# Kernel optimization log

Hardware: AMD Instinct MI355X
Metric: run time of the kernel (lower is better)

The kernel has to match this reference:

```python
import jax, jax.numpy as jnp
import numpy as np

NUM_CAPSULE = 16
DIM_CAPSULE = 64
ROUTINGS = 3
T_EPS = 1e-7


def setup_inputs() -> dict:
    key = jax.random.key(0)
    k1, k2 = jax.random.split(key)
    x = jax.random.normal(k1, (64, 512, 768), dtype=jnp.float32)
    # xavier-normal-ish init for W: [1, input_dim_capsule, num_capsule*dim_capsule]
    fan_in, fan_out = 768, NUM_CAPSULE * DIM_CAPSULE
    std = float(np.sqrt(2.0 / (fan_in + fan_out)))
    W = jax.random.normal(k2, (1, 768, NUM_CAPSULE * DIM_CAPSULE), dtype=jnp.float32) * std
    return {"x": x, "W": W}


def _squash(v, eps=T_EPS):
    # NOTE: this module's 'squash' is pure L2 normalization with eps, not the
    # classic (s^2/(1+s^2)) squash.
    s2 = jnp.sum(v * v, axis=-1, keepdims=True)
    return v / jnp.sqrt(s2 + eps)


def reference(x, W):
    B, In, _ = x.shape
    # u_hat: [B, In, num*dim] -> [B, num, In, dim]
    u = jnp.matmul(x, W).reshape(B, In, NUM_CAPSULE, DIM_CAPSULE).transpose(0, 2, 1, 3)
    b = jnp.zeros((B, NUM_CAPSULE, In), dtype=u.dtype)  # routing logits
    outputs = None
    for i in range(ROUTINGS):
        # torch code softmaxes over the num_capsule axis (after permute dance)
        c = jax.nn.softmax(b, axis=1)  # [B, num, In]
        outputs = _squash(jnp.einsum('bij,bijk->bik', c, u))  # [B, num, dim]
        if i < ROUTINGS - 1:
            b = jnp.einsum('bik,bijk->bij', outputs, u)  # [B, num, In]
    return outputs
```

## Files before the change

### kernel.cpp

```cpp
#include <hip/hip_runtime.h>
#include <hip/hip_bf16.h>
#include <stdint.h>

#define BATCH 64
#define IN_CAPS 512
#define NCAP 16
#define DCAP 64
#define GN (NCAP * DCAP)
#define GM (BATCH * IN_CAPS)
#define GK 768

typedef __bf16 bf16;
typedef __attribute__((ext_vector_type(8))) __bf16 bf16x8;
typedef __attribute__((ext_vector_type(4))) float f32x4;

__device__ inline void async16(const bf16* g, bf16* l) {
    __builtin_amdgcn_global_load_lds(
        (__attribute__((address_space(1))) void*)g,
        (__attribute__((address_space(3))) void*)l, 16, 0, 0);
}

__global__ __launch_bounds__(256) void k_convX2(const float* __restrict__ X,
                                                bf16* __restrict__ Xb,
                                                float* __restrict__ XS) {
    __shared__ float ls[GK];
    const int tid = threadIdx.x;
    ls[tid] = 0.f; ls[tid + 256] = 0.f; ls[tid + 512] = 0.f;
    __syncthreads();
    const size_t base = (size_t)blockIdx.x * (32 * GK);
    float acc[3][8] = {};
#pragma unroll
    for (int r = 0; r < 12; ++r) {
        const int off = r * 2048 + tid * 8;
        const f32x4 a0 = *(const f32x4*)(X + base + off);
        const f32x4 a1 = *(const f32x4*)(X + base + off + 4);
        bf16x8 o;
        o[0] = (bf16)a0[0]; o[1] = (bf16)a0[1]; o[2] = (bf16)a0[2]; o[3] = (bf16)a0[3];
        o[4] = (bf16)a1[0]; o[5] = (bf16)a1[1]; o[6] = (bf16)a1[2]; o[7] = (bf16)a1[3];
        *(bf16x8*)(Xb + base + off) = o;
        const int g = r % 3;
        acc[g][0] += a0[0]; acc[g][1] += a0[1];
        acc[g][2] += a0[2]; acc[g][3] += a0[3];
        acc[g][4] += a1[0]; acc[g][5] += a1[1];
        acc[g][6] += a1[2]; acc[g][7] += a1[3];
    }
    if (XS != nullptr) {
#pragma unroll
        for (int g = 0; g < 3; ++g) {
            const int cg = (g == 1) ? 512 : (g == 2) ? 256 : 0;
            const int kb = (tid * 8 + cg) % GK;
#pragma unroll
            for (int j = 0; j < 8; ++j) atomicAdd(&ls[kb + j], acc[g][j]);
        }
        __syncthreads();
        const int bidx = blockIdx.x >> 4;
        atomicAdd(&XS[(size_t)bidx * GK + tid],       ls[tid]);
        atomicAdd(&XS[(size_t)bidx * GK + tid + 256], ls[tid + 256]);
        atomicAdd(&XS[(size_t)bidx * GK + tid + 512], ls[tid + 512]);
    }
}

__global__ void k_transW(const float* __restrict__ W, bf16* __restrict__ Wt,
                         float* __restrict__ XS) {
    __shared__ bf16 t[32][33];
    const int k0 = blockIdx.x * 32;
    const int n0 = blockIdx.y * 32;
    const int tx = threadIdx.x, ty = threadIdx.y;
    if (XS != nullptr) {
        const int gid = (blockIdx.y * gridDim.x + blockIdx.x) * 256 + ty * 32 + tx;
        if (gid < BATCH * GK) XS[gid] = 0.f;
    }
#pragma unroll
    for (int r = 0; r < 4; ++r)
        t[ty + r * 8][tx] = (bf16)W[(size_t)(k0 + ty + r * 8) * GN + n0 + tx];
    __syncthreads();
#pragma unroll
    for (int r = 0; r < 4; ++r)
        Wt[(size_t)(n0 + ty + r * 8) * GK + k0 + tx] = t[tx][ty + r * 8];
}

__global__ __launch_bounds__(256) void k_out1(const float* __restrict__ XS,
                                              const float* __restrict__ W,
                                              float* __restrict__ O1) {
    __shared__ float xs[4][GK];
    __shared__ float red[4][4][64];
    const int cap = blockIdx.x & 15;
    const int bg = blockIdx.x >> 4;
    const int tid = threadIdx.x;
    const int k = tid & 63, kq = tid >> 6;
#pragma unroll
    for (int bb = 0; bb < 4; ++bb) {
        const size_t b = (size_t)(bg * 4 + bb);
        xs[bb][tid]       = XS[b * GK + tid];
        xs[bb][tid + 256] = XS[b * GK + tid + 256];
        xs[bb][tid + 512] = XS[b * GK + tid + 512];
    }
    __syncthreads();
    float acc4[4] = {0.f, 0.f, 0.f, 0.f};
    const float* wp = W + (size_t)(kq * 192) * GN + cap * 64 + k;
#pragma unroll 4
    for (int kk = 0; kk < 192; ++kk) {
        const float w = wp[(size_t)kk * GN];
        const int kx = kq * 192 + kk;
        acc4[0] += xs[0][kx] * w;
        acc4[1] += xs[1][kx] * w;
        acc4[2] += xs[2][kx] * w;
        acc4[3] += xs[3][kx] * w;
    }
#pragma unroll
    for (int bb = 0; bb < 4; ++bb) red[bb][kq][k] = acc4[bb];
    __syncthreads();
    if (tid < 64) {
#pragma unroll
        for (int bb = 0; bb < 4; ++bb) {
            float s = (red[bb][0][tid] + red[bb][1][tid] +
                       red[bb][2][tid] + red[bb][3][tid]) * 0.0625f;
            float ss = s * s;
#pragma unroll
            for (int off = 32; off >= 1; off >>= 1) ss += __shfl_xor(ss, off);
            O1[((size_t)(bg * 4 + bb) * NCAP + cap) * DCAP + tid] =
                s * rsqrtf(ss + 1e-7f);
        }
    }
}

__global__ __launch_bounds__(256) void k_gemm_frag(const bf16* __restrict__ Xb,
                                                   const bf16* __restrict__ Wt,
                                                   const float* __restrict__ O1,
                                                   bf16* __restrict__ U,
                                                   float* __restrict__ BL) {
    __shared__ bf16 sA[4096];
    __shared__ bf16 sB[4096];

    const int tid = threadIdx.x;
    const int lane = tid & 63;
    const int wave = tid >> 6;
    const int wm = wave >> 1, wn = wave & 1;
    const int m0 = blockIdx.x * 128;
    const int n0 = blockIdx.y * 128;

    const int r16 = lane & 15, q8 = (lane >> 4) * 8;
    const bf16* gA0 = Xb + (size_t)(m0 + wave * 16 + r16) * GK + q8;
    const bf16* gA1 = Xb + (size_t)(m0 + (wave + 4) * 16 + r16) * GK + q8;
    const bf16* gB0 = Wt + (size_t)(n0 + wave * 16 + r16) * GK + q8;
    const bf16* gB1 = Wt + (size_t)(n0 + (wave + 4) * 16 + r16) * GK + q8;

    f32x4 acc[4][4] = {};

    for (int kt = 0; kt < GK / 32; ++kt) {
        __syncthreads();
        async16(gA0, sA + wave * 512);
        async16(gA1, sA + (wave + 4) * 512);
        async16(gB0, sB + wave * 512);
        async16(gB1, sB + (wave + 4) * 512);
        gA0 += 32; gA1 += 32; gB0 += 32; gB1 += 32;
        __syncthreads();

        bf16x8 af[4], bv[4];
#pragma unroll
        for (int mi = 0; mi < 4; ++mi)
            af[mi] = *(const bf16x8*)(sA + (wm * 4 + mi) * 512 + lane * 8);
#pragma unroll
        for (int ni = 0; ni < 4; ++ni)
            bv[ni] = *(const bf16x8*)(sB + (wn * 4 + ni) * 512 + lane * 8);
#pragma unroll
        for (int mi = 0; mi < 4; ++mi)
#pragma unroll
            for (int ni = 0; ni < 4; ++ni)
                acc[mi][ni] = __builtin_amdgcn_mfma_f32_16x16x32_bf16(
                    af[mi], bv[ni], acc[mi][ni], 0, 0, 0);
    }

    const int fr = lane & 15;
    const int fq = lane >> 4;
#pragma unroll
    for (int mi = 0; mi < 4; ++mi) {
#pragma unroll
        for (int ni = 0; ni < 4; ++ni) {
#pragma unroll
            for (int r = 0; r < 4; ++r) {
                const int m = m0 + wm * 64 + mi * 16 + fq * 4 + r;
                const int n = n0 + wn * 64 + ni * 16 + fr;
                const int bb = m >> 9, j = m & 511;
                const int ci = n >> 6, k = n & 63;
                U[(((size_t)(bb * NCAP + ci)) * IN_CAPS + j) * DCAP + k] =
                    (bf16)acc[mi][ni][r];
            }
        }
    }

    if (O1 != nullptr) {
        const int b = m0 >> 9;
        const int cap = (n0 >> 6) + wn;
        float o1v[4];
#pragma unroll
        for (int ni = 0; ni < 4; ++ni)
            o1v[ni] = O1[(size_t)b * GN + n0 + wn * 64 + ni * 16 + fr];
#pragma unroll
        for (int mi = 0; mi < 4; ++mi) {
#pragma unroll
            for (int r = 0; r < 4; ++r) {
                float p = o1v[0] * acc[mi][0][r] + o1v[1] * acc[mi][1][r] +
                          o1v[2] * acc[mi][2][r] + o1v[3] * acc[mi][3][r];
                p += __shfl_xor(p, 1);
                p += __shfl_xor(p, 2);
                p += __shfl_xor(p, 4);
                p += __shfl_xor(p, 8);
                if (fr == 0) {
                    const int j = (m0 & 511) + wm * 64 + mi * 16 + fq * 4 + r;
                    BL[((size_t)(b * NCAP + cap)) * IN_CAPS + j] = p;
                }
            }
        }
    }
}

__global__ __launch_bounds__(256) void k_gemm_inline(const float* __restrict__ X,
                                                     const bf16* __restrict__ Wt,
                                                     bf16* __restrict__ U) {
    __shared__ bf16 sA[128 * 32];
    __shared__ bf16 sB[128 * 32];
    const int tid = threadIdx.x;
    const int lane = tid & 63;
    const int wave = tid >> 6;
    const int wm = wave >> 1, wn = wave & 1;
    const int m0 = blockIdx.x * 128;
    const int n0 = blockIdx.y * 128;
    const int srow = tid >> 2;
    const int scol = (tid & 3) * 8;
    f32x4 acc[4][4] = {};
    const int fr = lane & 15;
    const int fq = lane >> 4;
    for (int kt = 0; kt < GK / 32; ++kt) {
        const int kb = kt * 32;
        bf16x8 a0, a1, b0, b1;
        {
            const float* p = X + (size_t)(m0 + srow) * GK + kb + scol;
            const f32x4 x0 = *(const f32x4*)p, x1 = *(const f32x4*)(p + 4);
            const float* q = X + (size_t)(m0 + srow + 64) * GK + kb + scol;
            const f32x4 y0 = *(const f32x4*)q, y1 = *(const f32x4*)(q + 4);
#pragma unroll
            for (int c = 0; c < 4; ++c) {
                a0[c] = (bf16)x0[c]; a0[c + 4] = (bf16)x1[c];
                a1[c] = (bf16)y0[c]; a1[c + 4] = (bf16)y1[c];
            }
        }
        b0 = *(const bf16x8*)(Wt + (size_t)(n0 + srow) * GK + kb + scol);
        b1 = *(const bf16x8*)(Wt + (size_t)(n0 + srow + 64) * GK + kb + scol);
        __syncthreads();
        *(bf16x8*)(sA + srow * 32 + scol) = a0;
        *(bf16x8*)(sA + (srow + 64) * 32 + scol) = a1;
        *(bf16x8*)(sB + srow * 32 + scol) = b0;
        *(bf16x8*)(sB + (srow + 64) * 32 + scol) = b1;
        __syncthreads();
        bf16x8 af[4], bfr[4];
#pragma unroll
        for (int mi = 0; mi < 4; ++mi)
            af[mi] = *(const bf16x8*)(sA + (wm * 64 + mi * 16 + fr) * 32 + fq * 8);
#pragma unroll
        for (int ni = 0; ni < 4; ++ni)
            bfr[ni] = *(const bf16x8*)(sB + (wn * 64 + ni * 16 + fr) * 32 + fq * 8);
#pragma unroll
        for (int mi = 0; mi < 4; ++mi)
#pragma unroll
            for (int ni = 0; ni < 4; ++ni)
                acc[mi][ni] = __builtin_amdgcn_mfma_f32_16x16x32_bf16(
                    af[mi], bfr[ni], acc[mi][ni], 0, 0, 0);
    }
#pragma unroll
    for (int mi = 0; mi < 4; ++mi) {
#pragma unroll
        for (int ni = 0; ni < 4; ++ni) {
#pragma unroll
            for (int r = 0; r < 4; ++r) {
                const int m = m0 + wm * 64 + mi * 16 + fq * 4 + r;
                const int n = n0 + wn * 64 + ni * 16 + fr;
                const int bb = m >> 9, j = m & 511;
                const int ci = n >> 6, k = n & 63;
                U[(((size_t)(bb * NCAP + ci)) * IN_CAPS + j) * DCAP + k] =
                    (bf16)acc[mi][ni][r];
            }
        }
    }
}

__global__ __launch_bounds__(256) void k_route(const bf16* __restrict__ U,
                                               float* __restrict__ BL,
                                               float* __restrict__ OutC,
                                               int mode) {
    __shared__ bf16 su[IN_CAPS * DCAP];
    __shared__ float sc[IN_CAPS];
    __shared__ float red2[4][64];
    __shared__ float sout[64];
    const int bi = blockIdx.x;
    const int b = bi >> 4, cap = bi & 15;
    const int tid = threadIdx.x;
    const int lane = tid & 63;
    const int wave = tid >> 6;
    const size_t ubase = (size_t)bi * IN_CAPS * DCAP;

    if (mode == 0) {
        sc[tid] = 0.0625f;
        sc[tid + 256] = 0.0625f;
    } else {
#pragma unroll
        for (int h = 0; h < 2; ++h) {
            const int j = tid + h * 256;
            const float* p = BL + (size_t)b * NCAP * IN_CAPS + j;
            float v[16], mx = -1e30f;
#pragma unroll
            for (int i = 0; i < 16; ++i) {
                v[i] = p[(size_t)i * IN_CAPS];
                mx = fmaxf(mx, v[i]);
            }
            float s = 0.f;
#pragma unroll
            for (int i = 0; i < 16; ++i) s += __expf(v[i] - mx);
            sc[j] = __expf(v[cap] - mx) / s;
        }
    }
    __syncthreads();

    const int g = tid & 7;
    const int jr = tid >> 3;

    float acc[8] = {};
#pragma unroll
    for (int it = 0; it < 16; ++it) {
        const int j = it * 32 + jr;
        const bf16x8 v = *(const bf16x8*)(U + ubase + (size_t)it * 2048 + tid * 8);
        if (mode != 2) *(bf16x8*)(su + it * 2048 + tid * 8) = v;
        const float cv = sc[j];
#pragma unroll
        for (int c = 0; c < 8; ++c) acc[c] += cv * (float)v[c];
    }
#pragma unroll
    for (int c = 0; c < 8; ++c) {
        acc[c] += __shfl_xor(acc[c], 8);
        acc[c] += __shfl_xor(acc[c], 16);
        acc[c] += __shfl_xor(acc[c], 32);
    }
    if ((lane >> 3) == 0) {
#pragma unroll
        for (int c = 0; c < 8; ++c) red2[wave][lane * 8 + c] = acc[c];
    }
    __syncthreads();

    if (tid < 64) {
        float s = red2[0][tid] + red2[1][tid] + red2[2][tid] + red2[3][tid];
        float ss = s * s;
#pragma unroll
        for (int off = 32; off >= 1; off >>= 1) ss += __shfl_xor(ss, off);
        const float val = s * rsqrtf(ss + 1e-7f);
        sout[tid] = val;
        if (mode == 2) OutC[(size_t)bi * DCAP + tid] = val;
    }
    if (mode == 2) return;
    __syncthreads();

    const f32x4 o0 = *(const f32x4*)(sout + g * 8);
    const f32x4 o1 = *(const f32x4*)(sout + g * 8 + 4);
#pragma unroll
    for (int it = 0; it < 16; ++it) {
        const int j = it * 32 + jr;
        const bf16x8 v = *(const bf16x8*)(su + it * 2048 + tid * 8);
        float p = o0[0] * (float)v[0] + o0[1] * (float)v[1] +
                  o0[2] * (float)v[2] + o0[3] * (float)v[3] +
                  o1[0] * (float)v[4] + o1[1] * (float)v[5] +
                  o1[2] * (float)v[6] + o1[3] * (float)v[7];
        p += __shfl_xor(p, 1);
        p += __shfl_xor(p, 2);
        p += __shfl_xor(p, 4);
        if (g == 0) BL[((size_t)b * NCAP + cap) * IN_CAPS + j] = p;
    }
}

extern "C" void kernel_launch(void* const* d_in, const int* in_sizes, int n_in,
                              void* d_out, int out_size, void* d_ws, size_t ws_size,
                              hipStream_t stream) {
    const float* X = (const float*)d_in[0];
    const float* W = (const float*)d_in[1];
    float* OutC = (float*)d_out;

    const size_t u_bytes = (size_t)BATCH * NCAP * IN_CAPS * DCAP * sizeof(bf16);
    const size_t xb_bytes = (size_t)GM * GK * sizeof(bf16);
    const size_t wt_bytes = (size_t)GN * GK * sizeof(bf16);
    const size_t bl_bytes = (size_t)BATCH * NCAP * IN_CAPS * sizeof(float);
    const size_t xs_bytes = (size_t)BATCH * GK * sizeof(float);
    const size_t o1_bytes = (size_t)BATCH * GN * sizeof(float);
    char* ws = (char*)d_ws;

    const size_t need_full = u_bytes + xb_bytes + wt_bytes + bl_bytes + xs_bytes + o1_bytes;
    const size_t need_async = u_bytes + xb_bytes + wt_bytes + bl_bytes;
    const size_t need_small = u_bytes + wt_bytes + bl_bytes;

    bf16* U = (bf16*)ws;

    if (ws_size >= need_full) {
        bf16* Xb = (bf16*)(ws + u_bytes);
        bf16* Wt = (bf16*)(ws + u_bytes + xb_bytes);
        float* BL = (float*)(ws + u_bytes + xb_bytes + wt_bytes);
        float* XS = (float*)(ws + u_bytes + xb_bytes + wt_bytes + bl_bytes);
        float* O1 = (float*)(ws + u_bytes + xb_bytes + wt_bytes + bl_bytes + xs_bytes);
        k_transW<<<dim3(GK / 32, GN / 32), dim3(32, 8), 0, stream>>>(W, Wt, XS);
        k_convX2<<<GM / 32, 256, 0, stream>>>(X, Xb, XS);
        k_out1<<<256, 256, 0, stream>>>(XS, W, O1);
        k_gemm_frag<<<dim3(GM / 128, GN / 128), 256, 0, stream>>>(Xb, Wt, O1, U, BL);
        k_route<<<BATCH * NCAP, 256, 0, stream>>>(U, BL, OutC, 1);
        k_route<<<BATCH * NCAP, 256, 0, stream>>>(U, BL, OutC, 2);
    } else if (ws_size >= need_async) {
        bf16* Xb = (bf16*)(ws + u_bytes);
        bf16* Wt = (bf16*)(ws + u_bytes + xb_bytes);
        float* BL = (float*)(ws + u_bytes + xb_bytes + wt_bytes);
        k_transW<<<dim3(GK / 32, GN / 32), dim3(32, 8), 0, stream>>>(W, Wt, nullptr);
        k_convX2<<<GM / 32, 256, 0, stream>>>(X, Xb, nullptr);
        k_gemm_frag<<<dim3(GM / 128, GN / 128), 256, 0, stream>>>(Xb, Wt, nullptr, U, BL);
        k_route<<<BATCH * NCAP, 256, 0, stream>>>(U, BL, OutC, 0);
        k_route<<<BATCH * NCAP, 256, 0, stream>>>(U, BL, OutC, 1);
        k_route<<<BATCH * NCAP, 256, 0, stream>>>(U, BL, OutC, 2);
    } else if (ws_size >= need_small) {
        bf16* Wt = (bf16*)(ws + u_bytes);
        float* BL = (float*)(ws + u_bytes + wt_bytes);
        k_transW<<<dim3(GK / 32, GN / 32), dim3(32, 8), 0, stream>>>(W, Wt, nullptr);
        k_gemm_inline<<<dim3(GM / 128, GN / 128), 256, 0, stream>>>(X, Wt, U);
        k_route<<<BATCH * NCAP, 256, 0, stream>>>(U, BL, OutC, 0);
        k_route<<<BATCH * NCAP, 256, 0, stream>>>(U, BL, OutC, 1);
        k_route<<<BATCH * NCAP, 256, 0, stream>>>(U, BL, OutC, 2);
    }
}
```

Measured before the change: 330.8 us.

## Use row-major LDS tiles in GEMM and drop LDS staging of U in routing

The GEMM now loads each 16-row chunk with four lanes per row, so global reads are contiguous 64-byte row segments instead of fragment-ordered strided reads. MFMA operands are read from a row-major LDS tile (rows of 32 bf16), which may introduce LDS bank conflicts. The routing kernel no longer keeps a 64 KB copy of U in shared memory and instead rereads U from global memory (likely cache-resident) in its second pass. This raises occupancy at the cost of a second global read.

After: 295.7 us. 1.12x faster.

```diff
diff --git a/kernel.cpp b/kernel.cpp
--- a/kernel.cpp
+++ b/kernel.cpp
@@ -124,13 +124,13 @@
     }
 }
 
-__global__ __launch_bounds__(256) void k_gemm_frag(const bf16* __restrict__ Xb,
-                                                   const bf16* __restrict__ Wt,
-                                                   const float* __restrict__ O1,
-                                                   bf16* __restrict__ U,
-                                                   float* __restrict__ BL) {
-    __shared__ bf16 sA[4096];
-    __shared__ bf16 sB[4096];
+__global__ __launch_bounds__(256) void k_gemm_async(const bf16* __restrict__ Xb,
+                                                    const bf16* __restrict__ Wt,
+                                                    const float* __restrict__ O1,
+                                                    bf16* __restrict__ U,
+                                                    float* __restrict__ BL) {
+    __shared__ bf16 sA[128 * 32];
+    __shared__ bf16 sB[128 * 32];
 
     const int tid = threadIdx.x;
     const int lane = tid & 63;
@@ -139,40 +139,45 @@
     const int m0 = blockIdx.x * 128;
     const int n0 = blockIdx.y * 128;
 
-    const int r16 = lane & 15, q8 = (lane >> 4) * 8;
-    const bf16* gA0 = Xb + (size_t)(m0 + wave * 16 + r16) * GK + q8;
-    const bf16* gA1 = Xb + (size_t)(m0 + (wave + 4) * 16 + r16) * GK + q8;
-    const bf16* gB0 = Wt + (size_t)(n0 + wave * 16 + r16) * GK + q8;
-    const bf16* gB1 = Wt + (size_t)(n0 + (wave + 4) * 16 + r16) * GK + q8;
+    const int c0 = wave * 2, c1 = wave * 2 + 1;
+    const int rl = lane >> 2, cl = (lane & 3) * 8;
+    const bf16* gA0 = Xb + (size_t)(m0 + c0 * 16 + rl) * GK + cl;
+    const bf16* gA1 = Xb + (size_t)(m0 + c1 * 16 + rl) * GK + cl;
+    const bf16* gB0 = Wt + (size_t)(n0 + c0 * 16 + rl) * GK + cl;
+    const bf16* gB1 = Wt + (size_t)(n0 + c1 * 16 + rl) * GK + cl;
+    bf16* lA0 = sA + c0 * 512;
+    bf16* lA1 = sA + c1 * 512;
+    bf16* lB0 = sB + c0 * 512;
+    bf16* lB1 = sB + c1 * 512;
 
     f32x4 acc[4][4] = {};
+    const int fr = lane & 15;
+    const int fq = lane >> 4;
 
     for (int kt = 0; kt < GK / 32; ++kt) {
         __syncthreads();
-        async16(gA0, sA + wave * 512);
-        async16(gA1, sA + (wave + 4) * 512);
-        async16(gB0, sB + wave * 512);
-        async16(gB1, sB + (wave + 4) * 512);
+        async16(gA0, lA0);
+        async16(gA1, lA1);
+        async16(gB0, lB0);
+        async16(gB1, lB1);
         gA0 += 32; gA1 += 32; gB0 += 32; gB1 += 32;
         __syncthreads();
 
-        bf16x8 af[4], bv[4];
+        bf16x8 af[4], bfr[4];
 #pragma unroll
         for (int mi = 0; mi < 4; ++mi)
-            af[mi] = *(const bf16x8*)(sA + (wm * 4 + mi) * 512 + lane * 8);
+            af[mi] = *(const bf16x8*)(sA + (wm * 64 + mi * 16 + fr) * 32 + fq * 8);
 #pragma unroll
         for (int ni = 0; ni < 4; ++ni)
-            bv[ni] = *(const bf16x8*)(sB + (wn * 4 + ni) * 512 + lane * 8);
+            bfr[ni] = *(const bf16x8*)(sB + (wn * 64 + ni * 16 + fr) * 32 + fq * 8);
 #pragma unroll
         for (int mi = 0; mi < 4; ++mi)
 #pragma unroll
             for (int ni = 0; ni < 4; ++ni)
                 acc[mi][ni] = __builtin_amdgcn_mfma_f32_16x16x32_bf16(
-                    af[mi], bv[ni], acc[mi][ni], 0, 0, 0);
-    }
-
-    const int fr = lane & 15;
-    const int fq = lane >> 4;
+                    af[mi], bfr[ni], acc[mi][ni], 0, 0, 0);
+    }
+
 #pragma unroll
     for (int mi = 0; mi < 4; ++mi) {
 #pragma unroll
@@ -288,7 +293,6 @@
                                                float* __restrict__ BL,
                                                float* __restrict__ OutC,
                                                int mode) {
-    __shared__ bf16 su[IN_CAPS * DCAP];
     __shared__ float sc[IN_CAPS];
     __shared__ float red2[4][64];
     __shared__ float sout[64];
@@ -329,7 +333,6 @@
     for (int it = 0; it < 16; ++it) {
         const int j = it * 32 + jr;
         const bf16x8 v = *(const bf16x8*)(U + ubase + (size_t)it * 2048 + tid * 8);
-        if (mode != 2) *(bf16x8*)(su + it * 2048 + tid * 8) = v;
         const float cv = sc[j];
 #pragma unroll
         for (int c = 0; c < 8; ++c) acc[c] += cv * (float)v[c];
@@ -363,7 +366,7 @@
 #pragma unroll
     for (int it = 0; it < 16; ++it) {
         const int j = it * 32 + jr;
-        const bf16x8 v = *(const bf16x8*)(su + it * 2048 + tid * 8);
+        const bf16x8 v = *(const bf16x8*)(U + ubase + (size_t)it * 2048 + tid * 8);
         float p = o0[0] * (float)v[0] + o0[1] * (float)v[1] +
                   o0[2] * (float)v[2] + o0[3] * (float)v[3] +
                   o1[0] * (float)v[4] + o1[1] * (float)v[5] +
@@ -405,7 +408,7 @@
         k_transW<<<dim3(GK / 32, GN / 32), dim3(32, 8), 0, stream>>>(W, Wt, XS);
         k_convX2<<<GM / 32, 256, 0, stream>>>(X, Xb, XS);
         k_out1<<<256, 256, 0, stream>>>(XS, W, O1);
-        k_gemm_frag<<<dim3(GM / 128, GN / 128), 256, 0, stream>>>(Xb, Wt, O1, U, BL);
+        k_gemm_async<<<dim3(GM / 128, GN / 128), 256, 0, stream>>>(Xb, Wt, O1, U, BL);
         k_route<<<BATCH * NCAP, 256, 0, stream>>>(U, BL, OutC, 1);
         k_route<<<BATCH * NCAP, 256, 0, stream>>>(U, BL, OutC, 2);
     } else if (ws_size >= need_async) {
@@ -414,7 +417,7 @@
         float* BL = (float*)(ws + u_bytes + xb_bytes + wt_bytes);
         k_transW<<<dim3(GK / 32, GN / 32), dim3(32, 8), 0, stream>>>(W, Wt, nullptr);
         k_convX2<<<GM / 32, 256, 0, stream>>>(X, Xb, nullptr);
-        k_gemm_frag<<<dim3(GM / 128, GN / 128), 256, 0, stream>>>(Xb, Wt, nullptr, U, BL);
+        k_gemm_async<<<dim3(GM / 128, GN / 128), 256, 0, stream>>>(Xb, Wt, nullptr, U, BL);
         k_route<<<BATCH * NCAP, 256, 0, stream>>>(U, BL, OutC, 0);
         k_route<<<BATCH * NCAP, 256, 0, stream>>>(U, BL, OutC, 1);
         k_route<<<BATCH * NCAP, 256, 0, stream>>>(U, BL, OutC, 2);
```
